# Performance work log

Measured on AMD Instinct MI355X. Metric: run time of the kernel, lower is better.

Reference implementation:

```python
import jax, jax.numpy as jnp
import numpy as np

EMBED, HEADS, LEVELS, POINTS = 256, 8, 4, 4
SPATIAL_SHAPES = np.array([[128, 128], [64, 64], [32, 32], [16, 16]], dtype=np.int32)


def _grid_init_bias():
    # Faithful reproduction of the sampling_offsets bias init (per-head directional grid).
    thetas = np.arange(HEADS, dtype=np.float32) * (2.0 * np.pi / HEADS)
    g = np.stack([np.cos(thetas), np.sin(thetas)], -1)
    g = g / np.abs(g).max(-1, keepdims=True)
    g = np.tile(g.reshape(HEADS, 1, 1, 2), (1, LEVELS, POINTS, 1))
    for i in range(POINTS):
        g[:, :, i, :] *= i + 1
    return g.reshape(-1).astype(np.float32)


def setup_inputs() -> dict:
    key = jax.random.key(0)
    ks = jax.random.split(key, 8)
    bs = 2
    V = int((SPATIAL_SHAPES[:, 0] * SPATIAL_SHAPES[:, 1]).sum())  # 21760
    Q = V  # encoder self-attention
    C = EMBED
    n_off = HEADS * LEVELS * POINTS * 2
    n_attn = HEADS * LEVELS * POINTS
    inv_sqrt_c = 1.0 / np.sqrt(C)
    return {
        "query": jax.random.normal(ks[0], (bs, Q, C), jnp.float32),
        "value": jax.random.normal(ks[1], (bs, V, C), jnp.float32),
        "reference_points": jax.random.uniform(ks[2], (bs, Q, LEVELS, 2), jnp.float32),
        "spatial_shapes": SPATIAL_SHAPES,  # static int array
        # learned parameters (torch Linear stored as [in, out]: y = x @ W + b)
        "W_off": jax.random.normal(ks[3], (C, n_off), jnp.float32) * 0.01,
        "b_off": jnp.asarray(_grid_init_bias()),
        "W_attn": jax.random.normal(ks[4], (C, n_attn), jnp.float32) * 0.02,
        "b_attn": jnp.zeros((n_attn,), jnp.float32),
        "W_v": jax.random.normal(ks[5], (C, C), jnp.float32) * inv_sqrt_c,
        "b_v": jnp.zeros((C,), jnp.float32),
        "W_out": jax.random.normal(ks[6], (C, C), jnp.float32) * inv_sqrt_c,
        "b_out": jnp.zeros((C,), jnp.float32),
    }


def _ms_deform_attn(query, value, reference_points, shapes,
                    W_off, b_off, W_attn, b_attn, W_v, b_v, W_out, b_out):
    bs, Q, C = query.shape
    d = C // HEADS
    # value projection -> [bs, heads, V, d]
    val = (value @ W_v + b_v).reshape(bs, -1, HEADS, d).transpose(0, 2, 1, 3)
    # sampling offsets and attention weights from query
    off = (query @ W_off + b_off).reshape(bs, Q, HEADS, LEVELS, POINTS, 2)
    attn = jax.nn.softmax(
        (query @ W_attn + b_attn).reshape(bs, Q, HEADS, LEVELS * POINTS), axis=-1
    ).reshape(bs, Q, HEADS, LEVELS, POINTS)
    # offset normalizer is (W, H) per level
    norm = jnp.asarray(np.stack([shapes[:, 1], shapes[:, 0]], -1), jnp.float32)  # [L,2]
    loc = reference_points[:, :, None, :, None, :] + off / norm[None, None, None, :, None, :]

    out = jnp.zeros((bs, HEADS, Q, d), query.dtype)
    start = 0
    for l in range(LEVELS):
        H, W = int(shapes[l, 0]), int(shapes[l, 1])
        v_l = val[:, :, start:start + H * W]  # [bs, heads, H*W, d]
        start += H * W
        loc_l = loc[:, :, :, l]    # [bs, Q, heads, P, 2] in [0,1]
        attn_l = attn[:, :, :, l]  # [bs, Q, heads, P]
        # grid_sample(align_corners=False, padding_mode='zeros') semantics
        g = 2.0 * loc_l - 1.0
        x = (g[..., 0] + 1.0) * 0.5 * W - 0.5
        y = (g[..., 1] + 1.0) * 0.5 * H - 0.5
        x0 = jnp.floor(x)
        y0 = jnp.floor(y)
        for dx in (0, 1):
            for dy in (0, 1):
                xi = x0 + dx
                yi = y0 + dy
                w = (1.0 - jnp.abs(x - xi)) * (1.0 - jnp.abs(y - yi))
                valid = (xi >= 0) & (xi <= W - 1) & (yi >= 0) & (yi <= H - 1)
                w = jnp.where(valid, w, 0.0) * attn_l  # fused corner + attention weight
                idx = (jnp.clip(yi, 0, H - 1).astype(jnp.int32) * W
                       + jnp.clip(xi, 0, W - 1).astype(jnp.int32))  # [bs,Q,heads,P]
                idx_t = jnp.transpose(idx, (0, 2, 1, 3)).reshape(bs, HEADS, Q * POINTS)
                vals = jnp.take_along_axis(v_l, idx_t[..., None], axis=2)
                vals = vals.reshape(bs, HEADS, Q, POINTS, d)
                out = out + jnp.einsum('bhqpd,bqhp->bhqd', vals, w)
    out = out.transpose(0, 2, 1, 3).reshape(bs, Q, C)  # heads-major channel layout
    return out @ W_out + b_out


def reference(query, value, reference_points, spatial_shapes,
              W_off, b_off, W_attn, b_attn, W_v, b_v, W_out, b_out):
    shapes = np.asarray(spatial_shapes)  # static
    return _ms_deform_attn(query, value, reference_points, shapes,
                           W_off, b_off, W_attn, b_attn, W_v, b_v, W_out, b_out)
```

## Files before the change

### kernel.cpp

```cpp
#include <hip/hip_runtime.h>
#include <math.h>

#define EMBED 256
#define HEADS 8
#define LEVELS 4
#define POINTS 4
#define QN 21760
#define BS 2
#define MTOT (BS * QN)

typedef __attribute__((ext_vector_type(8))) short bf16x8;
typedef __attribute__((ext_vector_type(4))) float f32x4;

__device__ inline ushort f2bf(float f) {
  union { float f; uint u; } v; v.f = f;
  uint r = (v.u + 0x7FFFu + ((v.u >> 16) & 1u)) >> 16;
  return (ushort)r;
}
__device__ inline float bflo(uint u) { union { uint u; float f; } v; v.u = u << 16; return v.f; }
__device__ inline float bfhi(uint u) { union { uint u; float f; } v; v.u = u & 0xFFFF0000u; return v.f; }
__device__ inline uint pk2(float lo, float hi) { return (uint)f2bf(lo) | ((uint)f2bf(hi) << 16); }

__global__ __launch_bounds__(256) void prep_w(const float* __restrict__ W,
                                              ushort* __restrict__ Wt, int N) {
  int idx = blockIdx.x * 256 + threadIdx.x;
  int n = idx >> 8, k = idx & 255;
  Wt[idx] = f2bf(W[(size_t)k * N + n]);
}

template<int MODE, bool A_F32>
__global__ __launch_bounds__(256) void gemm_mfma(
    const void* __restrict__ A, const ushort* __restrict__ Bt,
    const float* __restrict__ bias, void* __restrict__ Cout, int N) {
  __shared__ ushort As[128][40];
  __shared__ ushort Bs[128][40];
  const int t = threadIdx.x;
  const int wave = t >> 6, lane = t & 63;
  const int bm = blockIdx.y * 128, bn = blockIdx.x * 128;
  const int wm = (wave >> 1) * 64, wn = (wave & 1) * 64;
  const int l15 = lane & 15, l4 = lane >> 4;

  f32x4 acc[4][4];
#pragma unroll
  for (int i = 0; i < 4; ++i)
#pragma unroll
    for (int j = 0; j < 4; ++j) acc[i][j] = (f32x4){0.f, 0.f, 0.f, 0.f};

  for (int k0 = 0; k0 < 256; k0 += 32) {
    if (A_F32) {
      const float* Af = (const float*)A;
#pragma unroll
      for (int i = 0; i < 4; ++i) {
        int c = t + i * 256;
        int row = c >> 3, part = c & 7;
        float4 v = *(const float4*)&Af[(size_t)(bm + row) * 256 + k0 + part * 4];
        ushort4 hv; hv.x = f2bf(v.x); hv.y = f2bf(v.y); hv.z = f2bf(v.z); hv.w = f2bf(v.w);
        *(ushort4*)&As[row][part * 4] = hv;
      }
    } else {
      const ushort* Ah = (const ushort*)A;
#pragma unroll
      for (int i = 0; i < 2; ++i) {
        int c = t + i * 256;
        int row = c >> 2, part = c & 3;
        *(float4*)&As[row][part * 8] = *(const float4*)&Ah[(size_t)(bm + row) * 256 + k0 + part * 8];
      }
    }
#pragma unroll
    for (int i = 0; i < 2; ++i) {
      int c = t + i * 256;
      int row = c >> 2, part = c & 3;
      *(float4*)&Bs[row][part * 8] = *(const float4*)&Bt[(size_t)(bn + row) * 256 + k0 + part * 8];
    }
    __syncthreads();

    bf16x8 af[4], bfr[4];
#pragma unroll
    for (int mi = 0; mi < 4; ++mi) af[mi] = *(const bf16x8*)&As[wm + mi * 16 + l15][l4 * 8];
#pragma unroll
    for (int ni = 0; ni < 4; ++ni) bfr[ni] = *(const bf16x8*)&Bs[wn + ni * 16 + l15][l4 * 8];
#pragma unroll
    for (int mi = 0; mi < 4; ++mi)
#pragma unroll
      for (int ni = 0; ni < 4; ++ni)
        acc[mi][ni] = __builtin_amdgcn_mfma_f32_16x16x32_bf16(af[mi], bfr[ni], acc[mi][ni], 0, 0, 0);
    __syncthreads();
  }

#pragma unroll
  for (int mi = 0; mi < 4; ++mi) {
#pragma unroll
    for (int ni = 0; ni < 4; ++ni) {
      int col = bn + wn + ni * 16 + l15;
      float bv = bias[col];
#pragma unroll
      for (int r = 0; r < 4; ++r) {
        int row = bm + wm + mi * 16 + l4 * 4 + r;
        float v = acc[mi][ni][r] + bv;
        if (MODE == 0) {
          ((float*)Cout)[(size_t)row * N + col] = v;
        } else {
          int b = (row >= QN) ? 1 : 0;
          int vpos = row - b * QN;
          int h = col >> 5, c = col & 31;
          ((ushort*)Cout)[((size_t)(b * 8 + h) * QN + vpos) * 32 + c] = f2bf(v);
        }
      }
    }
  }
}

__global__ __launch_bounds__(256) void msda_sample(
    const ushort* __restrict__ val, const float* __restrict__ off,
    const float* __restrict__ logits, const float* __restrict__ ref,
    ushort* __restrict__ interm) {
  const int lsz[LEVELS]    = {128, 64, 32, 16};
  const int lstart[LEVELS] = {0, 16384, 20480, 21504};

  int h   = blockIdx.x & 7;
  int z   = blockIdx.x >> 3;
  int sub = threadIdx.x & 3;
  int bq  = z * 64 + (threadIdx.x >> 2);
  int b   = (bq >= QN) ? 1 : 0;

  const float* lg = logits + (size_t)bq * 128 + h * 16;
  float w[16];
  float m = -1e30f;
#pragma unroll
  for (int s = 0; s < 16; ++s) { w[s] = lg[s]; m = fmaxf(m, w[s]); }
  float sum = 0.f;
#pragma unroll
  for (int s = 0; s < 16; ++s) { w[s] = __expf(w[s] - m); sum += w[s]; }
  float inv = 1.f / sum;

  float of[32];
  const float* offp = off + (size_t)bq * 256 + h * 32;
#pragma unroll
  for (int s = 0; s < 32; ++s) of[s] = offp[s];
  float rf[8];
  const float* refp = ref + (size_t)bq * 8;
#pragma unroll
  for (int s = 0; s < 8; ++s) rf[s] = refp[s];

  const ushort* vb = val + ((size_t)(b * 8 + h) * QN) * 32 + sub * 8;

  float acc[8] = {0.f, 0.f, 0.f, 0.f, 0.f, 0.f, 0.f, 0.f};

#pragma unroll
  for (int l = 0; l < LEVELS; ++l) {
    const int   W = lsz[l];
    const float fW = (float)W;
    const int   base = lstart[l];
    const float rx = rf[l * 2 + 0], ry = rf[l * 2 + 1];
#pragma unroll
    for (int p = 0; p < POINTS; ++p) {
      float x = rx * fW + of[l * 8 + p * 2 + 0] - 0.5f;
      float y = ry * fW + of[l * 8 + p * 2 + 1] - 0.5f;
      float x0f = floorf(x), y0f = floorf(y);
      int   x0 = (int)x0f,   y0 = (int)y0f;
      float fx = x - x0f,    fy = y - y0f;
      float a = w[l * 4 + p] * inv;
      float w00 = (1.f - fx) * (1.f - fy) * a;
      float w10 = fx * (1.f - fy) * a;
      float w01 = (1.f - fx) * fy * a;
      float w11 = fx * fy * a;
      bool xv0 = (x0 >= 0) && (x0 < W);
      bool xv1 = (x0 + 1 >= 0) && (x0 + 1 < W);
      bool yv0 = (y0 >= 0) && (y0 < W);
      bool yv1 = (y0 + 1 >= 0) && (y0 + 1 < W);

      const ushort* r0 = vb + (size_t)(base + y0 * W) * 32;
      const ushort* r1 = r0 + (size_t)W * 32;
      if (yv0 && xv0) {
        uint4 u = *(const uint4*)(r0 + (size_t)x0 * 32);
        acc[0] += w00 * bflo(u.x); acc[1] += w00 * bfhi(u.x);
        acc[2] += w00 * bflo(u.y); acc[3] += w00 * bfhi(u.y);
        acc[4] += w00 * bflo(u.z); acc[5] += w00 * bfhi(u.z);
        acc[6] += w00 * bflo(u.w); acc[7] += w00 * bfhi(u.w);
      }
      if (yv0 && xv1) {
        uint4 u = *(const uint4*)(r0 + (size_t)(x0 + 1) * 32);
        acc[0] += w10 * bflo(u.x); acc[1] += w10 * bfhi(u.x);
        acc[2] += w10 * bflo(u.y); acc[3] += w10 * bfhi(u.y);
        acc[4] += w10 * bflo(u.z); acc[5] += w10 * bfhi(u.z);
        acc[6] += w10 * bflo(u.w); acc[7] += w10 * bfhi(u.w);
      }
      if (yv1 && xv0) {
        uint4 u = *(const uint4*)(r1 + (size_t)x0 * 32);
        acc[0] += w01 * bflo(u.x); acc[1] += w01 * bfhi(u.x);
        acc[2] += w01 * bflo(u.y); acc[3] += w01 * bfhi(u.y);
        acc[4] += w01 * bflo(u.z); acc[5] += w01 * bfhi(u.z);
        acc[6] += w01 * bflo(u.w); acc[7] += w01 * bfhi(u.w);
      }
      if (yv1 && xv1) {
        uint4 u = *(const uint4*)(r1 + (size_t)(x0 + 1) * 32);
        acc[0] += w11 * bflo(u.x); acc[1] += w11 * bfhi(u.x);
        acc[2] += w11 * bflo(u.y); acc[3] += w11 * bfhi(u.y);
        acc[4] += w11 * bflo(u.z); acc[5] += w11 * bfhi(u.z);
        acc[6] += w11 * bflo(u.w); acc[7] += w11 * bfhi(u.w);
      }
    }
  }

  uint4 o;
  o.x = pk2(acc[0], acc[1]); o.y = pk2(acc[2], acc[3]);
  o.z = pk2(acc[4], acc[5]); o.w = pk2(acc[6], acc[7]);
  ushort* ip = interm + (size_t)bq * 256 + h * 32 + sub * 8;
  *(uint4*)ip = o;
}

extern "C" void kernel_launch(void* const* d_in, const int* in_sizes, int n_in,
                              void* d_out, int out_size, void* d_ws, size_t ws_size,
                              hipStream_t stream) {
  const float* query = (const float*)d_in[0];
  const float* value = (const float*)d_in[1];
  const float* ref   = (const float*)d_in[2];
  const float* W_off  = (const float*)d_in[4];
  const float* b_off  = (const float*)d_in[5];
  const float* W_attn = (const float*)d_in[6];
  const float* b_attn = (const float*)d_in[7];
  const float* W_v    = (const float*)d_in[8];
  const float* b_v    = (const float*)d_in[9];
  const float* W_out  = (const float*)d_in[10];
  const float* b_out  = (const float*)d_in[11];
  float* out = (float*)d_out;

  const size_t szBQC = (size_t)MTOT * EMBED;

  ushort* ws_wv    = (ushort*)d_ws;
  ushort* ws_woff  = ws_wv + 65536;
  ushort* ws_wattn = ws_woff + 65536;
  ushort* ws_wout  = ws_wattn + 32768;
  ushort* ws_val   = ws_wout + 65536;
  ushort* ws_interm= ws_val + szBQC;
  float*  ws_off   = (float*)(ws_interm + szBQC);
  float*  ws_log   = ws_off + szBQC;
  size_t need = (size_t)(65536*3 + 32768) * 2 + 2 * szBQC * 2 + szBQC * 4 + (size_t)MTOT * 128 * 4;
  if (ws_size < need) return;

  dim3 blk(256);
  prep_w<<<dim3(256), blk, 0, stream>>>(W_v, ws_wv, 256);
  prep_w<<<dim3(256), blk, 0, stream>>>(W_off, ws_woff, 256);
  prep_w<<<dim3(128), blk, 0, stream>>>(W_attn, ws_wattn, 128);
  prep_w<<<dim3(256), blk, 0, stream>>>(W_out, ws_wout, 256);

  dim3 g256(2, MTOT / 128);
  dim3 g128(1, MTOT / 128);
  gemm_mfma<1, true><<<g256, blk, 0, stream>>>(value, ws_wv, b_v, ws_val, 256);
  gemm_mfma<0, true><<<g256, blk, 0, stream>>>(query, ws_woff, b_off, ws_off, 256);
  gemm_mfma<0, true><<<g128, blk, 0, stream>>>(query, ws_wattn, b_attn, ws_log, 128);
  msda_sample<<<dim3(680 * 8), blk, 0, stream>>>(ws_val, ws_off, ws_log, ref, ws_interm);
  gemm_mfma<0, false><<<g256, blk, 0, stream>>>(ws_interm, ws_wout, b_out, out, 256);
}
```

Before: 311.0 us.

## Pre-cast inputs to bf16, fuse offset/attn GEMMs, async LDS loads, branchless sampling

Query and value are cast to bf16 in separate passes. The GEMM then loads A and B tiles straight into LDS with global_load_lds instead of converting through registers. The offset and attention-logit projections are merged into one N=384 GEMM with a combined weight and bias, so the query is read once. The sampler clamps corner indices and zeroes invalid weights instead of branching, uses packed float2 accumulation, and buffers are aliased in the workspace. The extra cast kernels add a full read and write of query and value, and the LDS layout is now unpadded, which may cause bank conflicts.

```diff
diff --git a/kernel.cpp b/kernel.cpp
--- a/kernel.cpp
+++ b/kernel.cpp
@@ -11,6 +11,7 @@
 
 typedef __attribute__((ext_vector_type(8))) short bf16x8;
 typedef __attribute__((ext_vector_type(4))) float f32x4;
+typedef __attribute__((ext_vector_type(2))) float f32x2;
 
 __device__ inline ushort f2bf(float f) {
   union { float f; uint u; } v; v.f = f;
@@ -20,6 +21,23 @@
 __device__ inline float bflo(uint u) { union { uint u; float f; } v; v.u = u << 16; return v.f; }
 __device__ inline float bfhi(uint u) { union { uint u; float f; } v; v.u = u & 0xFFFF0000u; return v.f; }
 __device__ inline uint pk2(float lo, float hi) { return (uint)f2bf(lo) | ((uint)f2bf(hi) << 16); }
+
+__device__ inline void g2l(const ushort* g, ushort* l) {
+  __builtin_amdgcn_global_load_lds(
+      (const __attribute__((address_space(1))) void*)g,
+      (__attribute__((address_space(3))) void*)l, 16, 0, 0);
+}
+
+__global__ __launch_bounds__(256) void cast_bf16(const float* __restrict__ x,
+                                                 ushort* __restrict__ y) {
+  int i = blockIdx.x * 256 + threadIdx.x;
+  const float4* xp = (const float4*)x;
+  float4 a = xp[2 * i], b = xp[2 * i + 1];
+  uint4 o;
+  o.x = pk2(a.x, a.y); o.y = pk2(a.z, a.w);
+  o.z = pk2(b.x, b.y); o.w = pk2(b.z, b.w);
+  ((uint4*)y)[i] = o;
+}
 
 __global__ __launch_bounds__(256) void prep_w(const float* __restrict__ W,
                                               ushort* __restrict__ Wt, int N) {
@@ -28,18 +46,34 @@
   Wt[idx] = f2bf(W[(size_t)k * N + n]);
 }
 
-template<int MODE, bool A_F32>
-__global__ __launch_bounds__(256) void gemm_mfma(
-    const void* __restrict__ A, const ushort* __restrict__ Bt,
+__global__ __launch_bounds__(256) void prep_wofflog(
+    const float* __restrict__ Woff, const float* __restrict__ Wattn,
+    const float* __restrict__ boff, const float* __restrict__ battn,
+    ushort* __restrict__ Wt, float* __restrict__ biasf) {
+  int idx = blockIdx.x * 256 + threadIdx.x;
+  int n = idx >> 8, k = idx & 255;
+  float v = (n < 256) ? Woff[(size_t)k * 256 + n] : Wattn[(size_t)k * 128 + (n - 256)];
+  Wt[idx] = f2bf(v);
+  if (idx < 384) biasf[idx] = (idx < 256) ? boff[idx] : battn[idx - 256];
+}
+
+template<int MODE>
+__global__ __launch_bounds__(256) void gemm_bf16(
+    const ushort* __restrict__ A, const ushort* __restrict__ Bt,
     const float* __restrict__ bias, void* __restrict__ Cout, int N) {
-  __shared__ ushort As[128][40];
-  __shared__ ushort Bs[128][40];
-  const int t = threadIdx.x;
-  const int wave = t >> 6, lane = t & 63;
+  __shared__ ushort As[128 * 32];
+  __shared__ ushort Bs[128 * 32];
+  const int t = threadIdx.x, wave = t >> 6, lane = t & 63;
   const int bm = blockIdx.y * 128, bn = blockIdx.x * 128;
   const int wm = (wave >> 1) * 64, wn = (wave & 1) * 64;
   const int l15 = lane & 15, l4 = lane >> 4;
 
+  const int srow = lane >> 2, sch = lane & 3;
+  const ushort* Ag = A + (size_t)(bm + 32 * wave + srow) * 256 + sch * 8;
+  const ushort* Bg = Bt + (size_t)(bn + 32 * wave + srow) * 256 + sch * 8;
+  ushort* la = &As[(32 * wave) * 32];
+  ushort* lb = &Bs[(32 * wave) * 32];
+
   f32x4 acc[4][4];
 #pragma unroll
   for (int i = 0; i < 4; ++i)
@@ -47,44 +81,23 @@
     for (int j = 0; j < 4; ++j) acc[i][j] = (f32x4){0.f, 0.f, 0.f, 0.f};
 
   for (int k0 = 0; k0 < 256; k0 += 32) {
-    if (A_F32) {
-      const float* Af = (const float*)A;
-#pragma unroll
-      for (int i = 0; i < 4; ++i) {
-        int c = t + i * 256;
-        int row = c >> 3, part = c & 7;
-        float4 v = *(const float4*)&Af[(size_t)(bm + row) * 256 + k0 + part * 4];
-        ushort4 hv; hv.x = f2bf(v.x); hv.y = f2bf(v.y); hv.z = f2bf(v.z); hv.w = f2bf(v.w);
-        *(ushort4*)&As[row][part * 4] = hv;
-      }
-    } else {
-      const ushort* Ah = (const ushort*)A;
-#pragma unroll
-      for (int i = 0; i < 2; ++i) {
-        int c = t + i * 256;
-        int row = c >> 2, part = c & 3;
-        *(float4*)&As[row][part * 8] = *(const float4*)&Ah[(size_t)(bm + row) * 256 + k0 + part * 8];
-      }
-    }
-#pragma unroll
-    for (int i = 0; i < 2; ++i) {
-      int c = t + i * 256;
-      int row = c >> 2, part = c & 3;
-      *(float4*)&Bs[row][part * 8] = *(const float4*)&Bt[(size_t)(bn + row) * 256 + k0 + part * 8];
-    }
     __syncthreads();
+    g2l(Ag + k0, la);
+    g2l(Ag + 16 * 256 + k0, la + 16 * 32);
+    g2l(Bg + k0, lb);
+    g2l(Bg + 16 * 256 + k0, lb + 16 * 32);
+    __syncthreads();
 
     bf16x8 af[4], bfr[4];
 #pragma unroll
-    for (int mi = 0; mi < 4; ++mi) af[mi] = *(const bf16x8*)&As[wm + mi * 16 + l15][l4 * 8];
-#pragma unroll
-    for (int ni = 0; ni < 4; ++ni) bfr[ni] = *(const bf16x8*)&Bs[wn + ni * 16 + l15][l4 * 8];
+    for (int mi = 0; mi < 4; ++mi) af[mi] = *(const bf16x8*)&As[(wm + mi * 16 + l15) * 32 + l4 * 8];
+#pragma unroll
+    for (int ni = 0; ni < 4; ++ni) bfr[ni] = *(const bf16x8*)&Bs[(wn + ni * 16 + l15) * 32 + l4 * 8];
 #pragma unroll
     for (int mi = 0; mi < 4; ++mi)
 #pragma unroll
       for (int ni = 0; ni < 4; ++ni)
         acc[mi][ni] = __builtin_amdgcn_mfma_f32_16x16x32_bf16(af[mi], bfr[ni], acc[mi][ni], 0, 0, 0);
-    __syncthreads();
   }
 
 #pragma unroll
@@ -111,9 +124,8 @@
 }
 
 __global__ __launch_bounds__(256) void msda_sample(
-    const ushort* __restrict__ val, const float* __restrict__ off,
-    const float* __restrict__ logits, const float* __restrict__ ref,
-    ushort* __restrict__ interm) {
+    const ushort* __restrict__ val, const float* __restrict__ offlog,
+    const float* __restrict__ ref, ushort* __restrict__ interm) {
   const int lsz[LEVELS]    = {128, 64, 32, 16};
   const int lstart[LEVELS] = {0, 16384, 20480, 21504};
 
@@ -123,7 +135,7 @@
   int bq  = z * 64 + (threadIdx.x >> 2);
   int b   = (bq >= QN) ? 1 : 0;
 
-  const float* lg = logits + (size_t)bq * 128 + h * 16;
+  const float* lg = offlog + (size_t)bq * 384 + 256 + h * 16;
   float w[16];
   float m = -1e30f;
 #pragma unroll
@@ -133,80 +145,83 @@
   for (int s = 0; s < 16; ++s) { w[s] = __expf(w[s] - m); sum += w[s]; }
   float inv = 1.f / sum;
 
-  float of[32];
-  const float* offp = off + (size_t)bq * 256 + h * 32;
-#pragma unroll
-  for (int s = 0; s < 32; ++s) of[s] = offp[s];
-  float rf[8];
+  const float* offp = offlog + (size_t)bq * 384 + h * 32;
   const float* refp = ref + (size_t)bq * 8;
-#pragma unroll
-  for (int s = 0; s < 8; ++s) rf[s] = refp[s];
-
-  const ushort* vb = val + ((size_t)(b * 8 + h) * QN) * 32 + sub * 8;
-
-  float acc[8] = {0.f, 0.f, 0.f, 0.f, 0.f, 0.f, 0.f, 0.f};
+  const ushort* vb  = val + ((size_t)(b * 8 + h) * QN) * 32 + sub * 8;
+
+  f32x2 a0 = {0.f, 0.f}, a1 = {0.f, 0.f}, a2 = {0.f, 0.f}, a3 = {0.f, 0.f};
 
 #pragma unroll
   for (int l = 0; l < LEVELS; ++l) {
     const int   W = lsz[l];
     const float fW = (float)W;
     const int   base = lstart[l];
-    const float rx = rf[l * 2 + 0], ry = rf[l * 2 + 1];
+    const float rx = refp[l * 2 + 0], ry = refp[l * 2 + 1];
 #pragma unroll
     for (int p = 0; p < POINTS; ++p) {
-      float x = rx * fW + of[l * 8 + p * 2 + 0] - 0.5f;
-      float y = ry * fW + of[l * 8 + p * 2 + 1] - 0.5f;
+      float ox = offp[(l * 4 + p) * 2 + 0];
+      float oy = offp[(l * 4 + p) * 2 + 1];
+      float x = rx * fW + ox - 0.5f;
+      float y = ry * fW + oy - 0.5f;
       float x0f = floorf(x), y0f = floorf(y);
       int   x0 = (int)x0f,   y0 = (int)y0f;
       float fx = x - x0f,    fy = y - y0f;
       float a = w[l * 4 + p] * inv;
-      float w00 = (1.f - fx) * (1.f - fy) * a;
-      float w10 = fx * (1.f - fy) * a;
-      float w01 = (1.f - fx) * fy * a;
-      float w11 = fx * fy * a;
-      bool xv0 = (x0 >= 0) && (x0 < W);
-      bool xv1 = (x0 + 1 >= 0) && (x0 + 1 < W);
-      bool yv0 = (y0 >= 0) && (y0 < W);
-      bool yv1 = (y0 + 1 >= 0) && (y0 + 1 < W);
-
-      const ushort* r0 = vb + (size_t)(base + y0 * W) * 32;
-      const ushort* r1 = r0 + (size_t)W * 32;
-      if (yv0 && xv0) {
-        uint4 u = *(const uint4*)(r0 + (size_t)x0 * 32);
-        acc[0] += w00 * bflo(u.x); acc[1] += w00 * bfhi(u.x);
-        acc[2] += w00 * bflo(u.y); acc[3] += w00 * bfhi(u.y);
-        acc[4] += w00 * bflo(u.z); acc[5] += w00 * bfhi(u.z);
-        acc[6] += w00 * bflo(u.w); acc[7] += w00 * bfhi(u.w);
-      }
-      if (yv0 && xv1) {
-        uint4 u = *(const uint4*)(r0 + (size_t)(x0 + 1) * 32);
-        acc[0] += w10 * bflo(u.x); acc[1] += w10 * bfhi(u.x);
-        acc[2] += w10 * bflo(u.y); acc[3] += w10 * bfhi(u.y);
-        acc[4] += w10 * bflo(u.z); acc[5] += w10 * bfhi(u.z);
-        acc[6] += w10 * bflo(u.w); acc[7] += w10 * bfhi(u.w);
-      }
-      if (yv1 && xv0) {
-        uint4 u = *(const uint4*)(r1 + (size_t)x0 * 32);
-        acc[0] += w01 * bflo(u.x); acc[1] += w01 * bfhi(u.x);
-        acc[2] += w01 * bflo(u.y); acc[3] += w01 * bfhi(u.y);
-        acc[4] += w01 * bflo(u.z); acc[5] += w01 * bfhi(u.z);
-        acc[6] += w01 * bflo(u.w); acc[7] += w01 * bfhi(u.w);
-      }
-      if (yv1 && xv1) {
-        uint4 u = *(const uint4*)(r1 + (size_t)(x0 + 1) * 32);
-        acc[0] += w11 * bflo(u.x); acc[1] += w11 * bfhi(u.x);
-        acc[2] += w11 * bflo(u.y); acc[3] += w11 * bfhi(u.y);
-        acc[4] += w11 * bflo(u.z); acc[5] += w11 * bfhi(u.z);
-        acc[6] += w11 * bflo(u.w); acc[7] += w11 * bfhi(u.w);
+      int x0c = min(max(x0, 0), W - 1);
+      int x1c = min(max(x0 + 1, 0), W - 1);
+      int y0c = min(max(y0, 0), W - 1);
+      int y1c = min(max(y0 + 1, 0), W - 1);
+      float wx0 = (x0 >= 0 && x0 < W) ? (1.f - fx) : 0.f;
+      float wx1 = (x0 + 1 >= 0 && x0 + 1 < W) ? fx : 0.f;
+      float wy0 = (y0 >= 0 && y0 < W) ? (1.f - fy) : 0.f;
+      float wy1 = (y0 + 1 >= 0 && y0 + 1 < W) ? fy : 0.f;
+      float w00 = wx0 * wy0 * a, w10 = wx1 * wy0 * a;
+      float w01 = wx0 * wy1 * a, w11 = wx1 * wy1 * a;
+
+      const uint4* p00 = (const uint4*)(vb + (size_t)(base + y0c * W + x0c) * 32);
+      const uint4* p10 = (const uint4*)(vb + (size_t)(base + y0c * W + x1c) * 32);
+      const uint4* p01 = (const uint4*)(vb + (size_t)(base + y1c * W + x0c) * 32);
+      const uint4* p11 = (const uint4*)(vb + (size_t)(base + y1c * W + x1c) * 32);
+      uint4 u00 = *p00;
+      uint4 u10 = *p10;
+      uint4 u01 = *p01;
+      uint4 u11 = *p11;
+
+      {
+        f32x2 wv = {w00, w00}; f32x2 v;
+        v.x = bflo(u00.x); v.y = bfhi(u00.x); a0 += v * wv;
+        v.x = bflo(u00.y); v.y = bfhi(u00.y); a1 += v * wv;
+        v.x = bflo(u00.z); v.y = bfhi(u00.z); a2 += v * wv;
+        v.x = bflo(u00.w); v.y = bfhi(u00.w); a3 += v * wv;
+      }
+      {
+        f32x2 wv = {w10, w10}; f32x2 v;
+        v.x = bflo(u10.x); v.y = bfhi(u10.x); a0 += v * wv;
+        v.x = bflo(u10.y); v.y = bfhi(u10.y); a1 += v * wv;
+        v.x = bflo(u10.z); v.y = bfhi(u10.z); a2 += v * wv;
+        v.x = bflo(u10.w); v.y = bfhi(u10.w); a3 += v * wv;
+      }
+      {
+        f32x2 wv = {w01, w01}; f32x2 v;
+        v.x = bflo(u01.x); v.y = bfhi(u01.x); a0 += v * wv;
+        v.x = bflo(u01.y); v.y = bfhi(u01.y); a1 += v * wv;
+        v.x = bflo(u01.z); v.y = bfhi(u01.z); a2 += v * wv;
+        v.x = bflo(u01.w); v.y = bfhi(u01.w); a3 += v * wv;
+      }
+      {
+        f32x2 wv = {w11, w11}; f32x2 v;
+        v.x = bflo(u11.x); v.y = bfhi(u11.x); a0 += v * wv;
+        v.x = bflo(u11.y); v.y = bfhi(u11.y); a1 += v * wv;
+        v.x = bflo(u11.z); v.y = bfhi(u11.z); a2 += v * wv;
+        v.x = bflo(u11.w); v.y = bfhi(u11.w); a3 += v * wv;
       }
     }
   }
 
   uint4 o;
-  o.x = pk2(acc[0], acc[1]); o.y = pk2(acc[2], acc[3]);
-  o.z = pk2(acc[4], acc[5]); o.w = pk2(acc[6], acc[7]);
-  ushort* ip = interm + (size_t)bq * 256 + h * 32 + sub * 8;
-  *(uint4*)ip = o;
+  o.x = pk2(a0.x, a0.y); o.y = pk2(a1.x, a1.y);
+  o.z = pk2(a2.x, a2.y); o.w = pk2(a3.x, a3.y);
+  *(uint4*)(interm + (size_t)bq * 256 + h * 32 + sub * 8) = o;
 }
 
 extern "C" void kernel_launch(void* const* d_in, const int* in_sizes, int n_in,
@@ -227,28 +242,30 @@
 
   const size_t szBQC = (size_t)MTOT * EMBED;
 
-  ushort* ws_wv    = (ushort*)d_ws;
-  ushort* ws_woff  = ws_wv + 65536;
-  ushort* ws_wattn = ws_woff + 65536;
-  ushort* ws_wout  = ws_wattn + 32768;
-  ushort* ws_val   = ws_wout + 65536;
-  ushort* ws_interm= ws_val + szBQC;
-  float*  ws_off   = (float*)(ws_interm + szBQC);
-  float*  ws_log   = ws_off + szBQC;
-  size_t need = (size_t)(65536*3 + 32768) * 2 + 2 * szBQC * 2 + szBQC * 4 + (size_t)MTOT * 128 * 4;
+  char* wsb = (char*)d_ws;
+  ushort* ws_wv      = (ushort*)(wsb + 0);
+  ushort* ws_wofflog = (ushort*)(wsb + 131072);
+  ushort* ws_wout    = (ushort*)(wsb + 327680);
+  float*  ws_biasf   = (float*)(wsb + 458752);
+  ushort* ws_val     = (ushort*)(wsb + 462848);
+  ushort* ws_q       = (ushort*)(wsb + 22745088);
+  ushort* ws_interm  = ws_q;
+  ushort* ws_v       = (ushort*)(wsb + 45027328);
+  float*  ws_offlog  = (float*)(wsb + 45027328);
+  size_t need = 45027328 + 66846720;
   if (ws_size < need) return;
 
   dim3 blk(256);
+
   prep_w<<<dim3(256), blk, 0, stream>>>(W_v, ws_wv, 256);
-  prep_w<<<dim3(256), blk, 0, stream>>>(W_off, ws_woff, 256);
-  prep_w<<<dim3(128), blk, 0, stream>>>(W_attn, ws_wattn, 128);
   prep_w<<<dim3(256), blk, 0, stream>>>(W_out, ws_wout, 256);
-
-  dim3 g256(2, MTOT / 128);
-  dim3 g128(1, MTOT / 128);
-  gemm_mfma<1, true><<<g256, blk, 0, stream>>>(value, ws_wv, b_v, ws_val, 256);
-  gemm_mfma<0, true><<<g256, blk, 0, stream>>>(query, ws_woff, b_off, ws_off, 256);
-  gemm_mfma<0, true><<<g128, blk, 0, stream>>>(query, ws_wattn, b_attn, ws_log, 128);
-  msda_sample<<<dim3(680 * 8), blk, 0, stream>>>(ws_val, ws_off, ws_log, ref, ws_interm);
-  gemm_mfma<0, false><<<g256, blk, 0, stream>>>(ws_interm, ws_wout, b_out, out, 256);
-}
+  prep_wofflog<<<dim3(384), blk, 0, stream>>>(W_off, W_attn, b_off, b_attn, ws_wofflog, ws_biasf);
+
+  cast_bf16<<<dim3(szBQC / 8 / 256), blk, 0, stream>>>(query, ws_q);
+  cast_bf16<<<dim3(szBQC / 8 / 256), blk, 0, stream>>>(value, ws_v);
+
+  gemm_bf16<1><<<dim3(2, MTOT / 128), blk, 0, stream>>>(ws_v, ws_wv, b_v, ws_val, 256);
+  gemm_bf16<0><<<dim3(3, MTOT / 128), blk, 0, stream>>>(ws_q, ws_wofflog, ws_biasf, ws_offlog, 384);
+  msda_sample<<<dim3(680 * 8), blk, 0, stream>>>(ws_val, ws_offlog, ref, ws_interm);
+  gemm_bf16<0><<<dim3(2, MTOT / 128), blk, 0, stream>>>(ws_interm, ws_wout, b_out, out, 256);
+}
```

New measurement: 314.2 us. About the same (+1.0%).
